# Kernel optimization log

Hardware: AMD Instinct MI355X
Metric: run time of the kernel (lower is better)

## Reference

```python
import jax, jax.numpy as jnp
import numpy as np


def _dense_image_warp(image, flow):
    """Faithful JAX port of tfa.image.dense_image_warp.

    image: [B,H,W,C] float, flow: [B,H,W,2] float (flow[...,0]=dy, flow[...,1]=dx).
    query point (y,x) = grid(y,x) - flow; bilinear interp with TFA's clamping:
    floor clipped to [0, size-2], alpha clipped to [0,1].
    """
    B, H, W, C = image.shape
    gy, gx = jnp.meshgrid(
        jnp.arange(H, dtype=flow.dtype), jnp.arange(W, dtype=flow.dtype), indexing="ij"
    )
    qy = gy[None] - flow[..., 0]  # [B,H,W]
    qx = gx[None] - flow[..., 1]

    y0f = jnp.clip(jnp.floor(qy), 0.0, H - 2)
    x0f = jnp.clip(jnp.floor(qx), 0.0, W - 2)
    ay = jnp.clip(qy - y0f, 0.0, 1.0)[..., None]  # [B,H,W,1]
    ax = jnp.clip(qx - x0f, 0.0, 1.0)[..., None]

    y0 = y0f.astype(jnp.int32)
    x0 = x0f.astype(jnp.int32)
    b = jnp.arange(B, dtype=jnp.int32)[:, None, None]

    tl = image[b, y0, x0]          # top-left  [B,H,W,C]
    tr = image[b, y0, x0 + 1]      # top-right
    bl = image[b, y0 + 1, x0]      # bottom-left
    br = image[b, y0 + 1, x0 + 1]  # bottom-right

    top = tl + ax * (tr - tl)
    bot = bl + ax * (br - bl)
    return top + ay * (bot - top)


def setup_inputs() -> dict:
    key = jax.random.key(0)
    k1, k2 = jax.random.split(key)
    B, H, W, C = 8, 1024, 768, 3
    image = jax.random.normal(k1, (B, H, W, C), dtype=jnp.float32)
    # flow magnitudes of a few pixels, typical for appearance-flow warping
    flow = jax.random.normal(k2, (B, H, W, 2), dtype=jnp.float32) * 5.0
    return {"image": image, "flow": flow}


def reference(image, flow):
    return _dense_image_warp(image, flow)
```

## Files before the change

kernel.cpp:

```cpp
#include <hip/hip_runtime.h>


constexpr int B = 8;
constexpr int H = 1024;
constexpr int W = 768;
constexpr int C = 3;

constexpr int TY = 64, TX = 32;
constexpr int WIN_ROWS = 97;
constexpr int WIN_COLS = 64;
constexpr int ROW_CHUNKS = 49;
constexpr int WSF = ROW_CHUNKS * 4;
constexpr int CHUNKS = WIN_ROWS * ROW_CHUNKS;
constexpr int TILES_X = W / TX;
constexpr int TILES_Y = H / TY;
constexpr int TILES_PER_B = TILES_X * TILES_Y;

constexpr int NTHREADS = 1024;
constexpr int NWAVES = NTHREADS / 64;
constexpr int PX_PER_T = (TY * TX) / NTHREADS;

typedef float vfloat2 __attribute__((ext_vector_type(2)));
typedef float vfloat4 __attribute__((ext_vector_type(4)));
typedef float vfloat2_a4 __attribute__((ext_vector_type(2), aligned(4)));
typedef float vfloat4_a4 __attribute__((ext_vector_type(4), aligned(4)));

__global__ __launch_bounds__(NTHREADS, 8) void warp_kernel(
    const float* __restrict__ image,
    const float* __restrict__ flow,
    float* __restrict__ out)
{
    __shared__ float win[WIN_ROWS * WSF + 192];

    const int flat = blockIdx.x;
    const int b    = flat & 7;
    const int s    = flat >> 3;
    const int ty   = s / TILES_X;
    const int tx   = s - ty * TILES_X;
    const int Y0 = ty * TY, X0 = tx * TX;

    const int rowLo = min(max(Y0 - 16, 0), H - WIN_ROWS);
    const int colLo = min(max(X0 - 16, 0), W - WIN_COLS);

    const int lane = threadIdx.x & 63;
    const int wv   = threadIdx.x >> 6;

    const float* gwin = image + ((size_t)b * H + rowLo) * (W * C) + colLo * C;
#pragma unroll 1
    for (int j = wv; j * 64 < CHUNKS; j += NWAVES) {
        int ci = j * 64 + lane;
        if (ci >= CHUNKS) ci = CHUNKS - 1;
        const int r = ci / ROW_CHUNKS;
        int c = ci - r * ROW_CHUNKS;
        if (c > 47) c = 47;
        const float* g = gwin + (size_t)r * (W * C) + c * 4;
        __builtin_amdgcn_global_load_lds(
            (const __attribute__((address_space(1))) void*)g,
            (__attribute__((address_space(3))) void*)(win + (size_t)j * 256),
            16, 0, 0);
    }

    vfloat2 f[PX_PER_T];
#pragma unroll
    for (int k = 0; k < PX_PER_T; ++k) {
        const int p   = threadIdx.x + k * NTHREADS;
        const int py  = p >> 5;
        const int pxx = p & 31;
        const size_t pix = ((size_t)b * H + (Y0 + py)) * W + (X0 + pxx);
        f[k] = __builtin_nontemporal_load((const vfloat2*)flow + pix);
    }

    __syncthreads();

#pragma unroll
    for (int k = 0; k < PX_PER_T; ++k) {
        const int p   = threadIdx.x + k * NTHREADS;
        const int py  = p >> 5;
        const int pxx = p & 31;
        const int y = Y0 + py;
        const int x = X0 + pxx;
        const size_t pix = ((size_t)b * H + y) * W + x;

        const float qy = (float)y - f[k].x;
        const float qx = (float)x - f[k].y;

        float y0f = floorf(qy);
        float x0f = floorf(qx);
        y0f = fminf(fmaxf(y0f, 0.0f), (float)(H - 2));
        x0f = fminf(fmaxf(x0f, 0.0f), (float)(W - 2));
        const float ay = fminf(fmaxf(qy - y0f, 0.0f), 1.0f);
        const float ax = fminf(fmaxf(qx - x0f, 0.0f), 1.0f);

        const int y0 = (int)y0f;
        const int x0 = (int)x0f;

        float tl0, tl1, tl2, tr0, tr1, tr2, bl0, bl1, bl2, br0, br1, br2;

        const bool inwin = (y0 >= rowLo) & (y0 <= rowLo + WIN_ROWS - 2) &
                           (x0 >= colLo) & (x0 <= colLo + WIN_COLS - 2);
        if (inwin) {
            const float* t = &win[(y0 - rowLo) * WSF + (x0 - colLo) * C];
            tl0 = t[0]; tl1 = t[1]; tl2 = t[2];
            tr0 = t[3]; tr1 = t[4]; tr2 = t[5];
            const float* bo = t + WSF;
            bl0 = bo[0]; bl1 = bo[1]; bl2 = bo[2];
            br0 = bo[3]; br1 = bo[4]; br2 = bo[5];
        } else {
            const float* top = image + (((size_t)b * H + y0) * W + x0) * C;
            const float* bot = top + (size_t)W * C;
            const vfloat4 t4 = *(const vfloat4_a4*)top;
            const vfloat2 t2 = *(const vfloat2_a4*)(top + 4);
            const vfloat4 b4 = *(const vfloat4_a4*)bot;
            const vfloat2 b2 = *(const vfloat2_a4*)(bot + 4);
            tl0 = t4.x; tl1 = t4.y; tl2 = t4.z;
            tr0 = t4.w; tr1 = t2.x; tr2 = t2.y;
            bl0 = b4.x; bl1 = b4.y; bl2 = b4.z;
            br0 = b4.w; br1 = b2.x; br2 = b2.y;
        }

        const float tp0 = tl0 + ax * (tr0 - tl0);
        const float tp1 = tl1 + ax * (tr1 - tl1);
        const float tp2 = tl2 + ax * (tr2 - tl2);
        const float bo0 = bl0 + ax * (br0 - bl0);
        const float bo1 = bl1 + ax * (br1 - bl1);
        const float bo2 = bl2 + ax * (br2 - bl2);

        float* o = out + pix * C;
        __builtin_nontemporal_store(tp0 + ay * (bo0 - tp0), &o[0]);
        __builtin_nontemporal_store(tp1 + ay * (bo1 - tp1), &o[1]);
        __builtin_nontemporal_store(tp2 + ay * (bo2 - tp2), &o[2]);
    }
}

extern "C" void kernel_launch(void* const* d_in, const int* in_sizes, int n_in,
                              void* d_out, int out_size, void* d_ws, size_t ws_size,
                              hipStream_t stream) {
    const float* image = (const float*)d_in[0];
    const float* flow  = (const float*)d_in[1];
    float* out = (float*)d_out;

    dim3 grid(B * TILES_PER_B);
    dim3 block(NTHREADS);
    warp_kernel<<<grid, block, 0, stream>>>(image, flow, out);
}
```

Before: 177.2 us.

## Vectorize flow loads and output stores with 4 pixels per thread, halve block size

New measurement: 181.8 us. 1.03x slower.

```diff
diff --git a/kernel.cpp b/kernel.cpp
--- a/kernel.cpp
+++ b/kernel.cpp
@@ -9,28 +9,28 @@
 constexpr int TY = 64, TX = 32;
 constexpr int WIN_ROWS = 97;
 constexpr int WIN_COLS = 64;
-constexpr int ROW_CHUNKS = 49;
-constexpr int WSF = ROW_CHUNKS * 4;
+constexpr int WSF = WIN_COLS * C;
+constexpr int ROW_CHUNKS = WSF / 4;
 constexpr int CHUNKS = WIN_ROWS * ROW_CHUNKS;
 constexpr int TILES_X = W / TX;
 constexpr int TILES_Y = H / TY;
 constexpr int TILES_PER_B = TILES_X * TILES_Y;
 
-constexpr int NTHREADS = 1024;
+constexpr int NTHREADS = 512;
 constexpr int NWAVES = NTHREADS / 64;
-constexpr int PX_PER_T = (TY * TX) / NTHREADS;
+constexpr int PXX = 4;
 
 typedef float vfloat2 __attribute__((ext_vector_type(2)));
 typedef float vfloat4 __attribute__((ext_vector_type(4)));
 typedef float vfloat2_a4 __attribute__((ext_vector_type(2), aligned(4)));
 typedef float vfloat4_a4 __attribute__((ext_vector_type(4), aligned(4)));
 
-__global__ __launch_bounds__(NTHREADS, 8) void warp_kernel(
+__global__ __launch_bounds__(NTHREADS, 4) void warp_kernel(
     const float* __restrict__ image,
     const float* __restrict__ flow,
     float* __restrict__ out)
 {
-    __shared__ float win[WIN_ROWS * WSF + 192];
+    __shared__ float win[WIN_ROWS * WSF + 64];
 
     const int flat = blockIdx.x;
     const int b    = flat & 7;
@@ -51,8 +51,7 @@
         int ci = j * 64 + lane;
         if (ci >= CHUNKS) ci = CHUNKS - 1;
         const int r = ci / ROW_CHUNKS;
-        int c = ci - r * ROW_CHUNKS;
-        if (c > 47) c = 47;
+        const int c = ci - r * ROW_CHUNKS;
         const float* g = gwin + (size_t)r * (W * C) + c * 4;
         __builtin_amdgcn_global_load_lds(
             (const __attribute__((address_space(1))) void*)g,
@@ -60,29 +59,25 @@
             16, 0, 0);
     }
 
-    vfloat2 f[PX_PER_T];
-#pragma unroll
-    for (int k = 0; k < PX_PER_T; ++k) {
-        const int p   = threadIdx.x + k * NTHREADS;
-        const int py  = p >> 5;
-        const int pxx = p & 31;
-        const size_t pix = ((size_t)b * H + (Y0 + py)) * W + (X0 + pxx);
-        f[k] = __builtin_nontemporal_load((const vfloat2*)flow + pix);
-    }
+    const int pr  = threadIdx.x >> 3;
+    const int xo  = (threadIdx.x & 7) * 4;
+    const int y   = Y0 + pr;
+    const int x   = X0 + xo;
+    const size_t pix = ((size_t)b * H + y) * W + x;
+
+    const vfloat4 fA = __builtin_nontemporal_load((const vfloat4*)(flow + pix * 2));
+    const vfloat4 fB = __builtin_nontemporal_load((const vfloat4*)(flow + pix * 2) + 1);
 
     __syncthreads();
 
+    const float fy[PXX] = {fA.x, fA.z, fB.x, fB.z};
+    const float fx[PXX] = {fA.y, fA.w, fB.y, fB.w};
+
+    float res[PXX][3];
 #pragma unroll
-    for (int k = 0; k < PX_PER_T; ++k) {
-        const int p   = threadIdx.x + k * NTHREADS;
-        const int py  = p >> 5;
-        const int pxx = p & 31;
-        const int y = Y0 + py;
-        const int x = X0 + pxx;
-        const size_t pix = ((size_t)b * H + y) * W + x;
-
-        const float qy = (float)y - f[k].x;
-        const float qx = (float)x - f[k].y;
+    for (int k = 0; k < PXX; ++k) {
+        const float qy = (float)y       - fy[k];
+        const float qx = (float)(x + k) - fx[k];
 
         float y0f = floorf(qy);
         float x0f = floorf(qx);
@@ -125,11 +120,18 @@
         const float bo1 = bl1 + ax * (br1 - bl1);
         const float bo2 = bl2 + ax * (br2 - bl2);
 
-        float* o = out + pix * C;
-        __builtin_nontemporal_store(tp0 + ay * (bo0 - tp0), &o[0]);
-        __builtin_nontemporal_store(tp1 + ay * (bo1 - tp1), &o[1]);
-        __builtin_nontemporal_store(tp2 + ay * (bo2 - tp2), &o[2]);
+        res[k][0] = tp0 + ay * (bo0 - tp0);
+        res[k][1] = tp1 + ay * (bo1 - tp1);
+        res[k][2] = tp2 + ay * (bo2 - tp2);
     }
+
+    const vfloat4 o0 = {res[0][0], res[0][1], res[0][2], res[1][0]};
+    const vfloat4 o1 = {res[1][1], res[1][2], res[2][0], res[2][1]};
+    const vfloat4 o2 = {res[2][2], res[3][0], res[3][1], res[3][2]};
+    vfloat4* o = (vfloat4*)(out + pix * C);
+    __builtin_nontemporal_store(o0, o + 0);
+    __builtin_nontemporal_store(o1, o + 1);
+    __builtin_nontemporal_store(o2, o + 2);
 }
 
 extern "C" void kernel_launch(void* const* d_in, const int* in_sizes, int n_in,
```
